# Performance work log

Hardware: AMD Instinct MI355X
Metric: run time of the kernel (lower is better)

## Reference

```python
import jax, jax.numpy as jnp
import numpy as np

N = 100000
C = 128
VEC = 16
GRID = 128
TEMP = 1.0
REP = C // VEC


def _offsets_cube():
    r = [-1, 0, 1]
    return np.array([[i, j, k] for i in r for j in r for k in r], dtype=np.int64)


def _offsets_cross(d):
    offs = [[0, 0, 0]]
    for ax in range(3):
        for s in (-d, d):
            o = [0, 0, 0]
            o[ax] = s
            offs.append(o)
    return np.array(offs, dtype=np.int64)


def _build_nbr(coords, lut, offs):
    # coords [N,3] int, lut: flat grid -> voxel idx or -1. Returns [K,N] int32, -1 = missing.
    maps = []
    for o in offs:
        nc = coords + o
        valid = np.all((nc >= 0) & (nc < GRID), axis=1)
        flat = nc[:, 0] * GRID * GRID + nc[:, 1] * GRID + nc[:, 2]
        idx = np.where(valid, lut[np.clip(flat, 0, GRID ** 3 - 1)], -1)
        maps.append(idx)
    return jnp.asarray(np.stack(maps).astype(np.int32))


def setup_inputs() -> dict:
    rng = np.random.default_rng(0)
    flat = rng.choice(GRID ** 3, size=N, replace=False)
    coords = np.stack([flat // (GRID * GRID), (flat // GRID) % GRID, flat % GRID], axis=1)
    lut = np.full(GRID ** 3, -1, dtype=np.int64)
    lut[flat] = np.arange(N)
    nbr_cross2 = _build_nbr(coords, lut, _offsets_cross(2))  # expert 0: HYPER_CROSS dil=2, K=7
    nbr_cube = _build_nbr(coords, lut, _offsets_cube())       # expert 1: HYPER_CUBE dil=1, K=27
    nbr_cross3 = _build_nbr(coords, lut, _offsets_cross(3))  # expert 2: HYPER_CROSS dil=3, K=7

    ks = jax.random.split(jax.random.key(0), 10)
    s = lambda k, shape, sc: jax.random.normal(k, shape, jnp.float32) * sc
    return dict(
        x=s(ks[0], (N, C), 1.0),
        v1_w=s(ks[1], (27, C, C), 0.05),
        v1_g=jnp.ones((C,), jnp.float32), v1_b=jnp.zeros((C,), jnp.float32),
        v2_w=s(ks[2], (C, C), 0.05),
        v2_g=jnp.ones((C,), jnp.float32), v2_b=jnp.zeros((C,), jnp.float32),
        q_w=s(ks[3], (C, VEC), 0.05),
        q_g=jnp.ones((VEC,), jnp.float32), q_b=jnp.zeros((VEC,), jnp.float32),
        cb0=s(ks[4], (7, C), 0.1),
        cb1=s(ks[5], (27, C), 0.1),
        cb2=s(ks[6], (7, C), 0.1),
        out_w=s(ks[7], (C, C), 0.05),
        out_g=jnp.ones((C,), jnp.float32), out_b=jnp.zeros((C,), jnp.float32),
        nbr_cross2=nbr_cross2, nbr_cube=nbr_cube, nbr_cross3=nbr_cross3,
    )


def _bn(x, g, b, eps=1e-5):
    m = x.mean(0)
    v = x.var(0)
    return (x - m) * jax.lax.rsqrt(v + eps) * g + b


def _sparse_conv(x, nbr, W):
    # full sparse conv: out[i] = sum_k W[k] @ x[nbr[k,i]] over valid neighbors
    out = jnp.zeros((x.shape[0], W.shape[2]), x.dtype)
    for k in range(W.shape[0]):  # fixed small K, structural loop
        idx = nbr[k]
        g = jnp.where((idx >= 0)[:, None], x[jnp.clip(idx, 0)], 0.0)
        out = out + g @ W[k]
    return out


def _chanwise_conv(x, nbr, kern):
    # MinkowskiChannelwiseConvolution: out[i,c] = sum_k kern[k,c] * x[nbr[k,i],c]
    out = jnp.zeros_like(x)
    for k in range(kern.shape[0]):
        idx = nbr[k]
        out = out + jnp.where((idx >= 0)[:, None], x[jnp.clip(idx, 0)], 0.0) * kern[k]
    return out


def _pairwise_score(q, nbr):
    # pairwise qk: mean over valid neighbors j of q_i * q_j (per channel) -> [N, VEC]
    acc = jnp.zeros_like(q)
    cnt = jnp.zeros((q.shape[0], 1), q.dtype)
    for k in range(nbr.shape[0]):
        idx = nbr[k]
        valid = (idx >= 0)[:, None]
        acc = acc + jnp.where(valid, q[jnp.clip(idx, 0)], 0.0)
        cnt = cnt + valid.astype(q.dtype)
    return q * acc / jnp.maximum(cnt, 1.0)


def reference(x, v1_w, v1_g, v1_b, v2_w, v2_g, v2_b, q_w, q_g, q_b,
              cb0, cb1, cb2, out_w, out_g, out_b,
              nbr_cross2, nbr_cube, nbr_cross3):
    # value branch: 3x3 ConvBNReLU -> 1x1 ConvBNReLU
    v = jax.nn.relu(_bn(_sparse_conv(x, nbr_cube, v1_w), v1_g, v1_b))
    v = jax.nn.relu(_bn(v @ v2_w, v2_g, v2_b))
    # query: 1x1 ConvBNReLU -> [N, VEC]
    q = jax.nn.relu(_bn(x @ q_w, q_g, q_b))
    # M=3 channelwise codebook expert convs on the value features
    cb_outs = [
        _chanwise_conv(v, nbr_cross2, cb0),
        _chanwise_conv(v, nbr_cube, cb1),
        _chanwise_conv(v, nbr_cross3, cb2),
    ]
    # pairwise attention scores per expert neighborhood -> [N, VEC, M]
    scores = jnp.stack([
        _pairwise_score(q, nbr_cross2),
        _pairwise_score(q, nbr_cube),
        _pairwise_score(q, nbr_cross3),
    ], axis=-1)
    attn = jax.nn.softmax(scores / TEMP, axis=-1)
    attn = jnp.repeat(attn, REP, axis=1)  # expand_vec_dim: [N, C, M]
    out = sum(attn[:, :, m] * cb_outs[m] for m in range(3))
    out = jax.nn.relu(_bn(out @ out_w, out_g, out_b))
    return out + x  # residual (inplanes == planes, downsample is identity)
```

## Files before the change

kernel.cpp:

```cpp
#include <hip/hip_runtime.h>

#define NN 100000
#define C 128
#define VEC 16
#define AROW 136
#define GCAP 240000

typedef __bf16 bfx8 __attribute__((ext_vector_type(8)));
typedef float f32x4 __attribute__((ext_vector_type(4)));

__device__ inline unsigned pack_bf2(float a, float b) {
    unsigned ua = __float_as_uint(a);
    unsigned ub = __float_as_uint(b);
    ua = (ua + 0x7fffu + ((ua >> 16) & 1u)) >> 16;
    ub = (ub + 0x7fffu + ((ub >> 16) & 1u)) >> 16;
    return ua | (ub << 16);
}
__device__ inline unsigned short bf1(float a) {
    unsigned u = __float_as_uint(a);
    return (unsigned short)((u + 0x7fffu + ((u >> 16) & 1u)) >> 16);
}

__device__ inline void wconv_body(const float* __restrict__ W, unsigned short* __restrict__ Wf, int F) {
    int e = F & 7, l = (F >> 3) & 63, nt = (F >> 9) & 7, ks = (F >> 12) & 3, kt = F >> 14;
    int cin = ks * 32 + (l >> 4) * 8 + e;
    int cout = nt * 16 + (l & 15);
    Wf[F] = bf1(W[((size_t)kt * C + cin) * C + cout]);
}

__global__ __launch_bounds__(256) void prep(const float* __restrict__ v1w, const float* __restrict__ v2w,
                                            const float* __restrict__ outw, const float* __restrict__ x,
                                            unsigned short* __restrict__ v1f, unsigned short* __restrict__ v2f,
                                            unsigned short* __restrict__ outf, unsigned short* __restrict__ xh) {
    int b = blockIdx.x, tid = threadIdx.x;
    if (b < 1728)       wconv_body(v1w, v1f, b * 256 + tid);
    else if (b < 1792)  wconv_body(v2w, v2f, (b - 1728) * 256 + tid);
    else if (b < 1856)  wconv_body(outw, outf, (b - 1792) * 256 + tid);
    else {
        const int total8 = NN * C / 8;
        for (int t = (b - 1856) * 256 + tid; t < total8; t += 1024 * 256) {
            float4 xa = *reinterpret_cast<const float4*>(x + (size_t)t * 8);
            float4 xb = *reinterpret_cast<const float4*>(x + (size_t)t * 8 + 4);
            uint4 pk;
            pk.x = pack_bf2(xa.x, xa.y); pk.y = pack_bf2(xa.z, xa.w);
            pk.z = pack_bf2(xb.x, xb.y); pk.w = pack_bf2(xb.z, xb.w);
            *reinterpret_cast<uint4*>(&xh[(size_t)t * 8]) = pk;
        }
    }
}

__global__ __launch_bounds__(256) void compactA(const int* __restrict__ nbr, int* __restrict__ cnt,
                                                int* __restrict__ slotmap, int* __restrict__ pairs,
                                                unsigned* __restrict__ maskbuf) {
    const int k = blockIdx.x / 49, cb = blockIdx.x % 49, tid = threadIdx.x;
    const int i0 = cb * 2048 + tid * 8;
    int j[8]; int lc = 0;
#pragma unroll
    for (int t = 0; t < 8; ++t) {
        int i = i0 + t;
        j[t] = (i < NN) ? nbr[(size_t)k * NN + i] : -1;
        lc += (j[t] >= 0);
    }
    __shared__ int ls[256]; __shared__ int sbase;
    ls[tid] = lc; __syncthreads();
    for (int off = 1; off < 256; off <<= 1) {
        int v = (tid >= off) ? ls[tid - off] : 0;
        __syncthreads();
        ls[tid] += v;
        __syncthreads();
    }
    if (tid == 255) sbase = atomicAdd(&cnt[k], ls[255]);
    __syncthreads();
    int slot = sbase + ls[tid] - lc;
    for (int t = 0; t < 8; ++t) {
        int i = i0 + t; if (i >= NN) break;
        int s = -1;
        if (j[t] >= 0) {
            s = slot++;
            pairs[(size_t)k * NN + s] = j[t];
            atomicOr(&maskbuf[i], 1u << k);
        }
        slotmap[(size_t)k * NN + i] = s;
    }
}

__global__ void prefixA2(int* __restrict__ hdr) {
    if (threadIdx.x == 0) {
        int co = 0, go = 0;
        for (int k = 0; k < 27; ++k) {
            hdr[32 + k] = co; hdr[64 + k] = go;
            int nch = (hdr[k] + 31) / 32;
            co += nch; go += nch * 32;
        }
        hdr[32 + 27] = co;
    }
}

__global__ __launch_bounds__(256) void convB(const unsigned short* __restrict__ xh, const int* __restrict__ pairs,
                                             const int* __restrict__ hdr, const bfx8* __restrict__ Wf,
                                             unsigned short* __restrict__ g) {
    const int tid = threadIdx.x, l = tid & 63, w = tid >> 6, rr = tid >> 4, gg = tid & 15;
    __shared__ int sco[28], scnt[27], sgo[27];
    __shared__ unsigned short Ash[32 * AROW];
    __shared__ unsigned short Osh[32 * AROW];
    if (tid < 28) sco[tid] = hdr[32 + tid];
    if (tid < 27) { scnt[tid] = hdr[tid]; sgo[tid] = hdr[64 + tid]; }
    __syncthreads();
    const int tot = sco[27];
    for (int t = blockIdx.x; t < tot; t += gridDim.x) {
        int lo = 0, hi = 26;
        while (lo < hi) { int mid = (lo + hi + 1) >> 1; if (sco[mid] <= t) lo = mid; else hi = mid - 1; }
        const int k = lo, c = t - sco[k], cntk = scnt[k];
        const int srow = c * 32;
        const size_t gbase = (size_t)(sgo[k] + srow) * C;
#pragma unroll
        for (int h = 0; h < 2; ++h) {
            int row = srow + h * 16 + rr;
            uint4 pk = {0u, 0u, 0u, 0u};
            if (row < cntk) {
                int j = pairs[(size_t)k * NN + row];
                pk = *reinterpret_cast<const uint4*>(xh + (size_t)j * C + gg * 8);
            }
            *reinterpret_cast<uint4*>(&Ash[(h * 16 + rr) * AROW + gg * 8]) = pk;
        }
        __syncthreads();
        f32x4 a00 = {0.f,0.f,0.f,0.f}, a01 = {0.f,0.f,0.f,0.f};
        f32x4 a10 = {0.f,0.f,0.f,0.f}, a11 = {0.f,0.f,0.f,0.f};
        const unsigned short* ar0 = &Ash[(l & 15) * AROW + (l >> 4) * 8];
        const unsigned short* ar1 = &Ash[(16 + (l & 15)) * AROW + (l >> 4) * 8];
#pragma unroll
        for (int ks = 0; ks < 4; ++ks) {
            bfx8 b0 = Wf[((k * 4 + ks) * 8 + 2 * w) * 64 + l];
            bfx8 b1 = Wf[((k * 4 + ks) * 8 + 2 * w + 1) * 64 + l];
            bfx8 f0 = *reinterpret_cast<const bfx8*>(ar0 + ks * 32);
            bfx8 f1 = *reinterpret_cast<const bfx8*>(ar1 + ks * 32);
            a00 = __builtin_amdgcn_mfma_f32_16x16x32_bf16(f0, b0, a00, 0, 0, 0);
            a01 = __builtin_amdgcn_mfma_f32_16x16x32_bf16(f0, b1, a01, 0, 0, 0);
            a10 = __builtin_amdgcn_mfma_f32_16x16x32_bf16(f1, b0, a10, 0, 0, 0);
            a11 = __builtin_amdgcn_mfma_f32_16x16x32_bf16(f1, b1, a11, 0, 0, 0);
        }
#pragma unroll
        for (int r = 0; r < 4; ++r) {
            int row = (l >> 4) * 4 + r;
            Osh[row * AROW + w * 32 + (l & 15)]        = bf1(a00[r]);
            Osh[row * AROW + w * 32 + 16 + (l & 15)]   = bf1(a01[r]);
            Osh[(16 + row) * AROW + w * 32 + (l & 15)] = bf1(a10[r]);
            Osh[(16 + row) * AROW + w * 32 + 16 + (l & 15)] = bf1(a11[r]);
        }
        __syncthreads();
#pragma unroll
        for (int h = 0; h < 2; ++h) {
            int row = h * 16 + rr;
            uint4 v = *reinterpret_cast<uint4*>(&Osh[row * AROW + gg * 8]);
            *reinterpret_cast<uint4*>(&g[gbase + (size_t)row * C + gg * 8]) = v;
        }
        __syncthreads();
    }
}

__global__ __launch_bounds__(256) void convC(const unsigned short* __restrict__ g, const int* __restrict__ slotmap,
                                             const int* __restrict__ hdr, const unsigned* __restrict__ maskbuf,
                                             unsigned short* __restrict__ outh, float* __restrict__ psb,
                                             float* __restrict__ pqb) {
    const int tid = threadIdx.x, p = tid >> 4, gg = tid & 15, c0 = gg * 8;
    const int i = blockIdx.x * 16 + p;
    __shared__ int sgo[27];
    __shared__ float outt[16 * 132];
    if (tid < 27) sgo[tid] = hdr[64 + tid];
    __syncthreads();
    unsigned m = maskbuf[i];
    float acc[8] = {0.f,0.f,0.f,0.f,0.f,0.f,0.f,0.f};
    while (m) {
        int k = (int)__builtin_ctz(m); m &= m - 1;
        int slot = slotmap[(size_t)k * NN + i];
        const unsigned short* gr = &g[(size_t)(sgo[k] + slot) * C + c0];
        uint4 u = *reinterpret_cast<const uint4*>(gr);
        acc[0] += __uint_as_float(u.x << 16); acc[1] += __uint_as_float(u.x & 0xffff0000u);
        acc[2] += __uint_as_float(u.y << 16); acc[3] += __uint_as_float(u.y & 0xffff0000u);
        acc[4] += __uint_as_float(u.z << 16); acc[5] += __uint_as_float(u.z & 0xffff0000u);
        acc[6] += __uint_as_float(u.w << 16); acc[7] += __uint_as_float(u.w & 0xffff0000u);
    }
#pragma unroll
    for (int c2 = 0; c2 < 8; ++c2) outt[p * 132 + c0 + c2] = acc[c2];
    uint4 pk;
    pk.x = pack_bf2(acc[0], acc[1]); pk.y = pack_bf2(acc[2], acc[3]);
    pk.z = pack_bf2(acc[4], acc[5]); pk.w = pack_bf2(acc[6], acc[7]);
    *reinterpret_cast<uint4*>(&outh[(size_t)i * C + c0]) = pk;
    __syncthreads();
    if (tid < 128) {
        float s = 0.f, q = 0.f;
#pragma unroll
        for (int r = 0; r < 16; ++r) { float v = outt[r * 132 + tid]; s += v; q += v * v; }
        psb[(size_t)blockIdx.x * C + tid] = s;
        pqb[(size_t)blockIdx.x * C + tid] = q;
    }
}

__global__ __launch_bounds__(256) void statsF128(const float* __restrict__ psb, const float* __restrict__ pqb,
                                                 int rows,
                                                 float* __restrict__ ps2, float* __restrict__ pq2,
                                                 const float* __restrict__ g, const float* __restrict__ b,
                                                 float* __restrict__ a, float* __restrict__ cc,
                                                 int* __restrict__ ticket) {
    const int tid = threadIdx.x, ch = tid & 127, half = tid >> 7;
    float s = 0.f, q = 0.f;
    for (int i = blockIdx.x * 2 + half; i < rows; i += 128) {
        s += psb[(size_t)i * C + ch];
        q += pqb[(size_t)i * C + ch];
    }
    __shared__ float ls[256], lq[256];
    __shared__ int amlast;
    ls[tid] = s; lq[tid] = q;
    __syncthreads();
    if (tid < 128) {
        ps2[blockIdx.x * C + ch] = ls[tid] + ls[tid + 128];
        pq2[blockIdx.x * C + ch] = lq[tid] + lq[tid + 128];
    }
    __threadfence();
    __syncthreads();
    if (tid == 0) amlast = (atomicAdd(ticket, 1) == 63) ? 1 : 0;
    __syncthreads();
    if (!amlast) return;
    __threadfence();
    if (tid < 128) {
        float ss = 0.f, qq = 0.f;
        for (int i = 0; i < 64; ++i) { ss += ps2[i * C + ch]; qq += pq2[i * C + ch]; }
        float m = ss / (float)NN;
        float var = fmaxf(qq / (float)NN - m * m, 0.f);
        float rs = rsqrtf(var + 1e-5f);
        float av = g[ch] * rs;
        a[ch] = av;
        cc[ch] = b[ch] - m * av;
    }
}

__global__ __launch_bounds__(256) void statsF16(const float* __restrict__ buf,
                                                float* __restrict__ ps2, float* __restrict__ pq2,
                                                const float* __restrict__ g, const float* __restrict__ b,
                                                float* __restrict__ a, float* __restrict__ cc,
                                                int* __restrict__ ticket) {
    const int tid = threadIdx.x, ch = tid & 15, grp = tid >> 4;
    float s = 0.f, q = 0.f;
    for (int i = blockIdx.x * 16 + grp; i < NN; i += 64 * 16) {
        float val = buf[(size_t)i * VEC + ch];
        s += val; q += val * val;
    }
    __shared__ float ls[256], lq[256];
    __shared__ int amlast;
    ls[tid] = s; lq[tid] = q;
    __syncthreads();
    if (tid < 16) {
        float ss = 0.f, qq = 0.f;
        for (int g2 = 0; g2 < 16; ++g2) { ss += ls[g2 * 16 + ch]; qq += lq[g2 * 16 + ch]; }
        ps2[blockIdx.x * VEC + ch] = ss; pq2[blockIdx.x * VEC + ch] = qq;
    }
    __threadfence();
    __syncthreads();
    if (tid == 0) amlast = (atomicAdd(ticket, 1) == 63) ? 1 : 0;
    __syncthreads();
    if (!amlast) return;
    __threadfence();
    if (tid < 16) {
        float ss = 0.f, qq = 0.f;
        for (int i = 0; i < 64; ++i) { ss += ps2[i * VEC + ch]; qq += pq2[i * VEC + ch]; }
        float m = ss / (float)NN;
        float var = fmaxf(qq / (float)NN - m * m, 0.f);
        float rs = rsqrtf(var + 1e-5f);
        float av = g[ch] * rs;
        a[ch] = av;
        cc[ch] = b[ch] - m * av;
    }
}

__global__ __launch_bounds__(256) void mm_bn_h32(const unsigned short* __restrict__ in,
                                                 const float* __restrict__ a,
                                                 const float* __restrict__ cc,
                                                 int dorelu,
                                                 const bfx8* __restrict__ Wf,
                                                 unsigned short* __restrict__ out,
                                                 float* __restrict__ psb,
                                                 float* __restrict__ pqb) {
    const int tid = threadIdx.x, l = tid & 63, w = tid >> 6;
    const int rr = tid >> 4, gg = tid & 15;
    const size_t base = (size_t)blockIdx.x * 32;
    __shared__ unsigned short Ash[32 * AROW];
    __shared__ float outt[32 * 132];
#pragma unroll
    for (int h = 0; h < 2; ++h) {
        int row = h * 16 + rr;
        uint4 u = *reinterpret_cast<const uint4*>(in + (base + row) * C + gg * 8);
        if (dorelu) {
            float4 a4 = *reinterpret_cast<const float4*>(&a[gg * 8]);
            float4 a4b = *reinterpret_cast<const float4*>(&a[gg * 8 + 4]);
            float4 c4 = *reinterpret_cast<const float4*>(&cc[gg * 8]);
            float4 c4b = *reinterpret_cast<const float4*>(&cc[gg * 8 + 4]);
            float e0 = fmaxf(fmaf(__uint_as_float(u.x << 16),        a4.x,  c4.x), 0.f);
            float e1 = fmaxf(fmaf(__uint_as_float(u.x & 0xffff0000u), a4.y,  c4.y), 0.f);
            float e2 = fmaxf(fmaf(__uint_as_float(u.y << 16),        a4.z,  c4.z), 0.f);
            float e3 = fmaxf(fmaf(__uint_as_float(u.y & 0xffff0000u), a4.w,  c4.w), 0.f);
            float e4 = fmaxf(fmaf(__uint_as_float(u.z << 16),        a4b.x, c4b.x), 0.f);
            float e5 = fmaxf(fmaf(__uint_as_float(u.z & 0xffff0000u), a4b.y, c4b.y), 0.f);
            float e6 = fmaxf(fmaf(__uint_as_float(u.w << 16),        a4b.z, c4b.z), 0.f);
            float e7 = fmaxf(fmaf(__uint_as_float(u.w & 0xffff0000u), a4b.w, c4b.w), 0.f);
            u.x = pack_bf2(e0, e1); u.y = pack_bf2(e2, e3);
            u.z = pack_bf2(e4, e5); u.w = pack_bf2(e6, e7);
        }
        *reinterpret_cast<uint4*>(&Ash[row * AROW + gg * 8]) = u;
    }
    __syncthreads();
    f32x4 a00 = {0.f,0.f,0.f,0.f}, a01 = {0.f,0.f,0.f,0.f};
    f32x4 a10 = {0.f,0.f,0.f,0.f}, a11 = {0.f,0.f,0.f,0.f};
    const unsigned short* ar0 = &Ash[(l & 15) * AROW + (l >> 4) * 8];
    const unsigned short* ar1 = &Ash[(16 + (l & 15)) * AROW + (l >> 4) * 8];
#pragma unroll
    for (int ks = 0; ks < 4; ++ks) {
        bfx8 b0 = Wf[(ks * 8 + 2 * w) * 64 + l];
        bfx8 b1 = Wf[(ks * 8 + 2 * w + 1) * 64 + l];
        bfx8 f0 = *reinterpret_cast<const bfx8*>(ar0 + ks * 32);
        bfx8 f1 = *reinterpret_cast<const bfx8*>(ar1 + ks * 32);
        a00 = __builtin_amdgcn_mfma_f32_16x16x32_bf16(f0, b0, a00, 0, 0, 0);
        a01 = __builtin_amdgcn_mfma_f32_16x16x32_bf16(f0, b1, a01, 0, 0, 0);
        a10 = __builtin_amdgcn_mfma_f32_16x16x32_bf16(f1, b0, a10, 0, 0, 0);
        a11 = __builtin_amdgcn_mfma_f32_16x16x32_bf16(f1, b1, a11, 0, 0, 0);
    }
#pragma unroll
    for (int r = 0; r < 4; ++r) {
        int row = (l >> 4) * 4 + r;
        outt[row * 132 + w * 32 + (l & 15)]        = a00[r];
        outt[row * 132 + w * 32 + 16 + (l & 15)]   = a01[r];
        outt[(16 + row) * 132 + w * 32 + (l & 15)] = a10[r];
        outt[(16 + row) * 132 + w * 32 + 16 + (l & 15)] = a11[r];
    }
    __syncthreads();
#pragma unroll
    for (int h = 0; h < 2; ++h) {
        int row = h * 16 + rr;
        float4 v0 = *reinterpret_cast<float4*>(&outt[row * 132 + gg * 8]);
        float4 v1 = *reinterpret_cast<float4*>(&outt[row * 132 + gg * 8 + 4]);
        uint4 pk;
        pk.x = pack_bf2(v0.x, v0.y); pk.y = pack_bf2(v0.z, v0.w);
        pk.z = pack_bf2(v1.x, v1.y); pk.w = pack_bf2(v1.z, v1.w);
        *reinterpret_cast<uint4*>(&out[(base + row) * C + gg * 8]) = pk;
    }
    if (tid < 128) {
        float s = 0.f, q = 0.f;
#pragma unroll
        for (int r = 0; r < 32; ++r) { float v = outt[r * 132 + tid]; s += v; q += v * v; }
        psb[(size_t)blockIdx.x * C + tid] = s;
        pqb[(size_t)blockIdx.x * C + tid] = q;
    }
}

__global__ __launch_bounds__(256) void qmm(const float* __restrict__ x,
                                           const float* __restrict__ qw,
                                           float* __restrict__ outq) {
    const int v = threadIdx.x & 15, p = threadIdx.x >> 4;
    const size_t i = (size_t)blockIdx.x * 16 + p;
    float acc = 0.f;
    for (int cin0 = 0; cin0 < C; cin0 += 4) {
        float4 xv = *reinterpret_cast<const float4*>(x + i * C + cin0);
        acc += xv.x * qw[(cin0 + 0) * VEC + v] + xv.y * qw[(cin0 + 1) * VEC + v]
             + xv.z * qw[(cin0 + 2) * VEC + v] + xv.w * qw[(cin0 + 3) * VEC + v];
    }
    outq[i * VEC + v] = acc;
}

__global__ __launch_bounds__(256) void attn_fused16e(const unsigned short* __restrict__ vraw,
                                                     const float* __restrict__ a2,
                                                     const float* __restrict__ c2,
                                                     const float* __restrict__ qraw,
                                                     const float* __restrict__ aq,
                                                     const float* __restrict__ cq,
                                                     const int* __restrict__ nA,
                                                     const int* __restrict__ nB,
                                                     const int* __restrict__ nC,
                                                     const float* __restrict__ cb0,
                                                     const float* __restrict__ cb1,
                                                     const float* __restrict__ cb2,
                                                     unsigned short* __restrict__ outm) {
    const int tid = threadIdx.x;
    const int base = blockIdx.x * 16;
    __shared__ int raw[16][41];
    __shared__ int sj[16][44];
    __shared__ short sk[16][44];
    __shared__ short sb[16][4];
    __shared__ float sattn[16][16][3];

    for (int t = tid; t < 656; t += 256) {
        int k = t >> 4, p = t & 15;
        int i = base + p;
        int j;
        if (k < 7)       j = nA[(size_t)k * NN + i];
        else if (k < 34) j = nB[(size_t)(k - 7) * NN + i];
        else             j = nC[(size_t)(k - 34) * NN + i];
        raw[p][k] = j;
    }
    __syncthreads();
    if (tid < 16) {
        int p = tid, n = 0;
#pragma unroll
        for (int k = 0; k < 7; ++k) { int j = raw[p][k]; if (j >= 0) { sj[p][n] = j; sk[p][n] = (short)k; ++n; } }
        int b0 = n;
#pragma unroll
        for (int k = 7; k < 34; ++k) { int j = raw[p][k]; if (j >= 0) { sj[p][n] = j; sk[p][n] = (short)(k - 7); ++n; } }
        int b1 = n;
#pragma unroll
        for (int k = 34; k < 41; ++k) { int j = raw[p][k]; if (j >= 0) { sj[p][n] = j; sk[p][n] = (short)(k - 34); ++n; } }
        sb[p][0] = (short)b0; sb[p][1] = (short)b1; sb[p][2] = (short)n;
    }
    __syncthreads();
    {
        int p = tid >> 4, v = tid & 15;
        int b0 = sb[p][0], b1 = sb[p][1], b2 = sb[p][2];
        float av = aq[v], cv = cq[v];
        float qi = fmaxf(fmaf(qraw[(size_t)(base + p) * VEC + v], av, cv), 0.f);
        float a0 = 0.f, a1 = 0.f, a2s = 0.f;
        for (int s = 0; s < b0; ++s) a0 += fmaxf(fmaf(qraw[(size_t)sj[p][s] * VEC + v], av, cv), 0.f);
        for (int s = b0; s < b1; ++s) a1 += fmaxf(fmaf(qraw[(size_t)sj[p][s] * VEC + v], av, cv), 0.f);
        for (int s = b1; s < b2; ++s) a2s += fmaxf(fmaf(qraw[(size_t)sj[p][s] * VEC + v], av, cv), 0.f);
        float s0 = qi * a0 / (float)(b0 > 0 ? b0 : 1);
        float s1 = qi * a1 / (float)(b1 - b0 > 0 ? b1 - b0 : 1);
        float s2 = qi * a2s / (float)(b2 - b1 > 0 ? b2 - b1 : 1);
        float mx = fmaxf(s0, fmaxf(s1, s2));
        float e0 = __expf(s0 - mx), e1 = __expf(s1 - mx), e2 = __expf(s2 - mx);
        float inv = 1.f / (e0 + e1 + e2);
        sattn[p][v][0] = e0 * inv; sattn[p][v][1] = e1 * inv; sattn[p][v][2] = e2 * inv;
    }
    __syncthreads();
    {
        int p = tid >> 4, g = tid & 15, c0 = g * 8;
        int b0 = sb[p][0], b1 = sb[p][1], b2 = sb[p][2];
        float4 va = *reinterpret_cast<const float4*>(&a2[c0]);
        float4 vab = *reinterpret_cast<const float4*>(&a2[c0 + 4]);
        float4 vc = *reinterpret_cast<const float4*>(&c2[c0]);
        float4 vcb = *reinterpret_cast<const float4*>(&c2[c0 + 4]);
        float A0[8], A1[8], A2[8];
#pragma unroll
        for (int c = 0; c < 8; ++c) { A0[c] = 0.f; A1[c] = 0.f; A2[c] = 0.f; }
        for (int s = 0; s < b0; ++s) {
            int j = sj[p][s], k = sk[p][s];
            uint4 u = *reinterpret_cast<const uint4*>(vraw + (size_t)j * C + c0);
            float4 ca = *reinterpret_cast<const float4*>(&cb0[k * C + c0]);
            float4 cb = *reinterpret_cast<const float4*>(&cb0[k * C + c0 + 4]);
            A0[0] = fmaf(ca.x, fmaxf(fmaf(__uint_as_float(u.x << 16),        va.x,  vc.x), 0.f), A0[0]);
            A0[1] = fmaf(ca.y, fmaxf(fmaf(__uint_as_float(u.x & 0xffff0000u), va.y,  vc.y), 0.f), A0[1]);
            A0[2] = fmaf(ca.z, fmaxf(fmaf(__uint_as_float(u.y << 16),        va.z,  vc.z), 0.f), A0[2]);
            A0[3] = fmaf(ca.w, fmaxf(fmaf(__uint_as_float(u.y & 0xffff0000u), va.w,  vc.w), 0.f), A0[3]);
            A0[4] = fmaf(cb.x, fmaxf(fmaf(__uint_as_float(u.z << 16),        vab.x, vcb.x), 0.f), A0[4]);
            A0[5] = fmaf(cb.y, fmaxf(fmaf(__uint_as_float(u.z & 0xffff0000u), vab.y, vcb.y), 0.f), A0[5]);
            A0[6] = fmaf(cb.z, fmaxf(fmaf(__uint_as_float(u.w << 16),        vab.z, vcb.z), 0.f), A0[6]);
            A0[7] = fmaf(cb.w, fmaxf(fmaf(__uint_as_float(u.w & 0xffff0000u), vab.w, vcb.w), 0.f), A0[7]);
        }
        for (int s = b0; s < b1; ++s) {
            int j = sj[p][s], k = sk[p][s];
            uint4 u = *reinterpret_cast<const uint4*>(vraw + (size_t)j * C + c0);
            float4 ca = *reinterpret_cast<const float4*>(&cb1[k * C + c0]);
            float4 cb = *reinterpret_cast<const float4*>(&cb1[k * C + c0 + 4]);
            A1[0] = fmaf(ca.x, fmaxf(fmaf(__uint_as_float(u.x << 16),        va.x,  vc.x), 0.f), A1[0]);
            A1[1] = fmaf(ca.y, fmaxf(fmaf(__uint_as_float(u.x & 0xffff0000u), va.y,  vc.y), 0.f), A1[1]);
            A1[2] = fmaf(ca.z, fmaxf(fmaf(__uint_as_float(u.y << 16),        va.z,  vc.z), 0.f), A1[2]);
            A1[3] = fmaf(ca.w, fmaxf(fmaf(__uint_as_float(u.y & 0xffff0000u), va.w,  vc.w), 0.f), A1[3]);
            A1[4] = fmaf(cb.x, fmaxf(fmaf(__uint_as_float(u.z << 16),        vab.x, vcb.x), 0.f), A1[4]);
            A1[5] = fmaf(cb.y, fmaxf(fmaf(__uint_as_float(u.z & 0xffff0000u), vab.y, vcb.y), 0.f), A1[5]);
            A1[6] = fmaf(cb.z, fmaxf(fmaf(__uint_as_float(u.w << 16),        vab.z, vcb.z), 0.f), A1[6]);
            A1[7] = fmaf(cb.w, fmaxf(fmaf(__uint_as_float(u.w & 0xffff0000u), vab.w, vcb.w), 0.f), A1[7]);
        }
        for (int s = b1; s < b2; ++s) {
            int j = sj[p][s], k = sk[p][s];
            uint4 u = *reinterpret_cast<const uint4*>(vraw + (size_t)j * C + c0);
            float4 ca = *reinterpret_cast<const float4*>(&cb2[k * C + c0]);
            float4 cb = *reinterpret_cast<const float4*>(&cb2[k * C + c0 + 4]);
            A2[0] = fmaf(ca.x, fmaxf(fmaf(__uint_as_float(u.x << 16),        va.x,  vc.x), 0.f), A2[0]);
            A2[1] = fmaf(ca.y, fmaxf(fmaf(__uint_as_float(u.x & 0xffff0000u), va.y,  vc.y), 0.f), A2[1]);
            A2[2] = fmaf(ca.z, fmaxf(fmaf(__uint_as_float(u.y << 16),        va.z,  vc.z), 0.f), A2[2]);
            A2[3] = fmaf(ca.w, fmaxf(fmaf(__uint_as_float(u.y & 0xffff0000u), va.w,  vc.w), 0.f), A2[3]);
            A2[4] = fmaf(cb.x, fmaxf(fmaf(__uint_as_float(u.z << 16),        vab.x, vcb.x), 0.f), A2[4]);
            A2[5] = fmaf(cb.y, fmaxf(fmaf(__uint_as_float(u.z & 0xffff0000u), vab.y, vcb.y), 0.f), A2[5]);
            A2[6] = fmaf(cb.z, fmaxf(fmaf(__uint_as_float(u.w << 16),        vab.z, vcb.z), 0.f), A2[6]);
            A2[7] = fmaf(cb.w, fmaxf(fmaf(__uint_as_float(u.w & 0xffff0000u), vab.w, vcb.w), 0.f), A2[7]);
        }
        float w0 = sattn[p][g][0], w1 = sattn[p][g][1], w2 = sattn[p][g][2];
        float o[8];
#pragma unroll
        for (int c = 0; c < 8; ++c) o[c] = w0 * A0[c] + w1 * A1[c] + w2 * A2[c];
        uint4 pk;
        pk.x = pack_bf2(o[0], o[1]); pk.y = pack_bf2(o[2], o[3]);
        pk.z = pack_bf2(o[4], o[5]); pk.w = pack_bf2(o[6], o[7]);
        *reinterpret_cast<uint4*>(&outm[(size_t)(base + p) * C + c0]) = pk;
    }
}

__global__ __launch_bounds__(256) void final_bn_res_h(const unsigned short* __restrict__ buf,
                                                      const float* __restrict__ a,
                                                      const float* __restrict__ cc,
                                                      const float* __restrict__ x,
                                                      float* __restrict__ out) {
    const int total8 = NN * C / 8;
    for (int t = blockIdx.x * 256 + threadIdx.x; t < total8; t += gridDim.x * 256) {
        int ch = (t * 8) & 127;
        uint4 u = *reinterpret_cast<const uint4*>(buf + (size_t)t * 8);
        float4 xa = *reinterpret_cast<const float4*>(x + (size_t)t * 8);
        float4 xb = *reinterpret_cast<const float4*>(x + (size_t)t * 8 + 4);
        float4 a4 = *reinterpret_cast<const float4*>(&a[ch]);
        float4 a4b = *reinterpret_cast<const float4*>(&a[ch + 4]);
        float4 c4 = *reinterpret_cast<const float4*>(&cc[ch]);
        float4 c4b = *reinterpret_cast<const float4*>(&cc[ch + 4]);
        float4 o0, o1;
        o0.x = fmaxf(fmaf(__uint_as_float(u.x << 16),        a4.x,  c4.x), 0.f) + xa.x;
        o0.y = fmaxf(fmaf(__uint_as_float(u.x & 0xffff0000u), a4.y,  c4.y), 0.f) + xa.y;
        o0.z = fmaxf(fmaf(__uint_as_float(u.y << 16),        a4.z,  c4.z), 0.f) + xa.z;
        o0.w = fmaxf(fmaf(__uint_as_float(u.y & 0xffff0000u), a4.w,  c4.w), 0.f) + xa.w;
        o1.x = fmaxf(fmaf(__uint_as_float(u.z << 16),        a4b.x, c4b.x), 0.f) + xb.x;
        o1.y = fmaxf(fmaf(__uint_as_float(u.z & 0xffff0000u), a4b.y, c4b.y), 0.f) + xb.y;
        o1.z = fmaxf(fmaf(__uint_as_float(u.w << 16),        a4b.z, c4b.z), 0.f) + xb.z;
        o1.w = fmaxf(fmaf(__uint_as_float(u.w & 0xffff0000u), a4b.w, c4b.w), 0.f) + xb.w;
        *reinterpret_cast<float4*>(out + (size_t)t * 8) = o0;
        *reinterpret_cast<float4*>(out + (size_t)t * 8 + 4) = o1;
    }
}

extern "C" void kernel_launch(void* const* d_in, const int* in_sizes, int n_in,
                              void* d_out, int out_size, void* d_ws, size_t ws_size,
                              hipStream_t stream) {
    (void)in_sizes; (void)n_in; (void)out_size; (void)ws_size;
    const float* x    = (const float*)d_in[0];
    const float* v1_w = (const float*)d_in[1];
    const float* v1_g = (const float*)d_in[2];
    const float* v1_b = (const float*)d_in[3];
    const float* v2_w = (const float*)d_in[4];
    const float* v2_g = (const float*)d_in[5];
    const float* v2_b = (const float*)d_in[6];
    const float* q_w  = (const float*)d_in[7];
    const float* q_g  = (const float*)d_in[8];
    const float* q_b  = (const float*)d_in[9];
    const float* cb0  = (const float*)d_in[10];
    const float* cb1  = (const float*)d_in[11];
    const float* cb2  = (const float*)d_in[12];
    const float* out_w = (const float*)d_in[13];
    const float* out_g = (const float*)d_in[14];
    const float* out_b = (const float*)d_in[15];
    const int* nbrA = (const int*)d_in[16];
    const int* nbrB = (const int*)d_in[17];
    const int* nbrC = (const int*)d_in[18];
    float* out = (float*)d_out;

    float* w = (float*)d_ws;
    unsigned short* bufAh = (unsigned short*)w;
    float* r1 = w + (size_t)NN * C / 2;
    unsigned short* g = (unsigned short*)r1;
    int* slotmap = (int*)(r1 + 15360000);
    int* pairs   = (int*)(r1 + 15360000 + 2700000);
    unsigned short* bufBh = (unsigned short*)r1;
    float* bufQ = r1 + 6400000;
    size_t o = (size_t)NN * C / 2 + 20760000;
    unsigned short* xh = (unsigned short*)(w + o); o += (size_t)NN * C / 2;
    float* psb  = w + o; o += (size_t)6250 * C;
    float* pqb  = w + o; o += (size_t)6250 * C;
    float* ps2  = w + o; o += 64 * C;
    float* pq2  = w + o; o += 64 * C;
    float* ps16 = w + o; o += 64 * VEC;
    float* pq16 = w + o; o += 64 * VEC;
    float* a1 = w + o; o += C;  float* c1 = w + o; o += C;
    float* a2 = w + o; o += C;  float* c2 = w + o; o += C;
    float* ao = w + o; o += C;  float* co = w + o; o += C;
    float* aq = w + o; o += VEC; float* cq = w + o; o += VEC;
    unsigned short* v1f = (unsigned short*)(w + o); o += (27 * 16384) / 2;
    unsigned short* v2f = (unsigned short*)(w + o); o += 16384 / 2;
    unsigned short* outf = (unsigned short*)(w + o); o += 16384 / 2;
    int* hdr = (int*)(w + o); o += 128;
    unsigned* maskbuf = (unsigned*)(w + o); o += NN;

    hipMemsetAsync(hdr, 0, (size_t)(128 + NN) * sizeof(int), stream);
    prep<<<2880, 256, 0, stream>>>(v1_w, v2_w, out_w, x, v1f, v2f, outf, xh);

    compactA<<<27 * 49, 256, 0, stream>>>(nbrB, hdr, slotmap, pairs, maskbuf);
    prefixA2<<<1, 64, 0, stream>>>(hdr);
    convB<<<2048, 256, 0, stream>>>(xh, pairs, hdr, (const bfx8*)v1f, g);
    convC<<<NN / 16, 256, 0, stream>>>(g, slotmap, hdr, maskbuf, bufAh, psb, pqb);
    statsF128<<<64, 256, 0, stream>>>(psb, pqb, 6250, ps2, pq2, v1_g, v1_b, a1, c1, hdr + 96);

    mm_bn_h32<<<NN / 32, 256, 0, stream>>>(bufAh, a1, c1, 1, (const bfx8*)v2f, bufBh, psb, pqb);
    statsF128<<<64, 256, 0, stream>>>(psb, pqb, 3125, ps2, pq2, v2_g, v2_b, a2, c2, hdr + 97);

    qmm<<<NN / 16, 256, 0, stream>>>(x, q_w, bufQ);
    statsF16<<<64, 256, 0, stream>>>(bufQ, ps16, pq16, q_g, q_b, aq, cq, hdr + 98);

    attn_fused16e<<<NN / 16, 256, 0, stream>>>(bufBh, a2, c2, bufQ, aq, cq,
                                               nbrA, nbrB, nbrC, cb0, cb1, cb2, bufAh);

    mm_bn_h32<<<NN / 32, 256, 0, stream>>>(bufAh, nullptr, nullptr, 0, (const bfx8*)outf, bufBh, psb, pqb);
    statsF128<<<64, 256, 0, stream>>>(psb, pqb, 3125, ps2, pq2, out_g, out_b, ao, co, hdr + 99);
    final_bn_res_h<<<2048, 256, 0, stream>>>(bufBh, ao, co, x, out);
}
```

Measured before the change: 338.0 us.

## Fuse output projection into attention kernel and fold prefix scan into compaction

The attention-mix kernel now multiplies its 16-row output tile by the output projection weights with MFMA and emits per-block BN partial sums directly. This removes the separate output matmul launch and the bf16 round-trip of the mixed features through global memory. The prefix computation over per-offset counts moves into the last-finishing compaction block via an atomic counter, and the query projection reads the bf16 copy of x instead of fp32. The costs are more shared memory per attention block, which may lower occupancy, and extra bf16 rounding of x in the query path.

```diff
diff --git a/kernel.cpp b/kernel.cpp
--- a/kernel.cpp
+++ b/kernel.cpp
@@ -49,7 +49,7 @@
     }
 }
 
-__global__ __launch_bounds__(256) void compactA(const int* __restrict__ nbr, int* __restrict__ cnt,
+__global__ __launch_bounds__(256) void compactA(const int* __restrict__ nbr, int* __restrict__ hdr,
                                                 int* __restrict__ slotmap, int* __restrict__ pairs,
                                                 unsigned* __restrict__ maskbuf) {
     const int k = blockIdx.x / 49, cb = blockIdx.x % 49, tid = threadIdx.x;
@@ -61,7 +61,7 @@
         j[t] = (i < NN) ? nbr[(size_t)k * NN + i] : -1;
         lc += (j[t] >= 0);
     }
-    __shared__ int ls[256]; __shared__ int sbase;
+    __shared__ int ls[256]; __shared__ int sbase; __shared__ int amlast;
     ls[tid] = lc; __syncthreads();
     for (int off = 1; off < 256; off <<= 1) {
         int v = (tid >= off) ? ls[tid - off] : 0;
@@ -69,7 +69,7 @@
         ls[tid] += v;
         __syncthreads();
     }
-    if (tid == 255) sbase = atomicAdd(&cnt[k], ls[255]);
+    if (tid == 255) sbase = atomicAdd(&hdr[k], ls[255]);
     __syncthreads();
     int slot = sbase + ls[tid] - lc;
     for (int t = 0; t < 8; ++t) {
@@ -82,17 +82,20 @@
         }
         slotmap[(size_t)k * NN + i] = s;
     }
-}
-
-__global__ void prefixA2(int* __restrict__ hdr) {
-    if (threadIdx.x == 0) {
+    __threadfence();
+    __syncthreads();
+    if (tid == 0) amlast = (atomicAdd(&hdr[100], 1) == 27 * 49 - 1) ? 1 : 0;
+    __syncthreads();
+    if (amlast && tid == 0) {
         int co = 0, go = 0;
-        for (int k = 0; k < 27; ++k) {
-            hdr[32 + k] = co; hdr[64 + k] = go;
-            int nch = (hdr[k] + 31) / 32;
+        for (int kk = 0; kk < 27; ++kk) {
+            int cnt = atomicAdd(&hdr[kk], 0);
+            hdr[32 + kk] = co; hdr[64 + kk] = go;
+            int nch = (cnt + 31) / 32;
             co += nch; go += nch * 32;
         }
         hdr[32 + 27] = co;
+        __threadfence();
     }
 }
 
@@ -275,7 +278,6 @@
 __global__ __launch_bounds__(256) void mm_bn_h32(const unsigned short* __restrict__ in,
                                                  const float* __restrict__ a,
                                                  const float* __restrict__ cc,
-                                                 int dorelu,
                                                  const bfx8* __restrict__ Wf,
                                                  unsigned short* __restrict__ out,
                                                  float* __restrict__ psb,
@@ -285,26 +287,24 @@
     const size_t base = (size_t)blockIdx.x * 32;
     __shared__ unsigned short Ash[32 * AROW];
     __shared__ float outt[32 * 132];
+    float4 a4 = *reinterpret_cast<const float4*>(&a[gg * 8]);
+    float4 a4b = *reinterpret_cast<const float4*>(&a[gg * 8 + 4]);
+    float4 c4 = *reinterpret_cast<const float4*>(&cc[gg * 8]);
+    float4 c4b = *reinterpret_cast<const float4*>(&cc[gg * 8 + 4]);
 #pragma unroll
     for (int h = 0; h < 2; ++h) {
         int row = h * 16 + rr;
         uint4 u = *reinterpret_cast<const uint4*>(in + (base + row) * C + gg * 8);
-        if (dorelu) {
-            float4 a4 = *reinterpret_cast<const float4*>(&a[gg * 8]);
-            float4 a4b = *reinterpret_cast<const float4*>(&a[gg * 8 + 4]);
-            float4 c4 = *reinterpret_cast<const float4*>(&cc[gg * 8]);
-            float4 c4b = *reinterpret_cast<const float4*>(&cc[gg * 8 + 4]);
-            float e0 = fmaxf(fmaf(__uint_as_float(u.x << 16),        a4.x,  c4.x), 0.f);
-            float e1 = fmaxf(fmaf(__uint_as_float(u.x & 0xffff0000u), a4.y,  c4.y), 0.f);
-            float e2 = fmaxf(fmaf(__uint_as_float(u.y << 16),        a4.z,  c4.z), 0.f);
-            float e3 = fmaxf(fmaf(__uint_as_float(u.y & 0xffff0000u), a4.w,  c4.w), 0.f);
-            float e4 = fmaxf(fmaf(__uint_as_float(u.z << 16),        a4b.x, c4b.x), 0.f);
-            float e5 = fmaxf(fmaf(__uint_as_float(u.z & 0xffff0000u), a4b.y, c4b.y), 0.f);
-            float e6 = fmaxf(fmaf(__uint_as_float(u.w << 16),        a4b.z, c4b.z), 0.f);
-            float e7 = fmaxf(fmaf(__uint_as_float(u.w & 0xffff0000u), a4b.w, c4b.w), 0.f);
-            u.x = pack_bf2(e0, e1); u.y = pack_bf2(e2, e3);
-            u.z = pack_bf2(e4, e5); u.w = pack_bf2(e6, e7);
-        }
+        float e0 = fmaxf(fmaf(__uint_as_float(u.x << 16),        a4.x,  c4.x), 0.f);
+        float e1 = fmaxf(fmaf(__uint_as_float(u.x & 0xffff0000u), a4.y,  c4.y), 0.f);
+        float e2 = fmaxf(fmaf(__uint_as_float(u.y << 16),        a4.z,  c4.z), 0.f);
+        float e3 = fmaxf(fmaf(__uint_as_float(u.y & 0xffff0000u), a4.w,  c4.w), 0.f);
+        float e4 = fmaxf(fmaf(__uint_as_float(u.z << 16),        a4b.x, c4b.x), 0.f);
+        float e5 = fmaxf(fmaf(__uint_as_float(u.z & 0xffff0000u), a4b.y, c4b.y), 0.f);
+        float e6 = fmaxf(fmaf(__uint_as_float(u.w << 16),        a4b.z, c4b.z), 0.f);
+        float e7 = fmaxf(fmaf(__uint_as_float(u.w & 0xffff0000u), a4b.w, c4b.w), 0.f);
+        u.x = pack_bf2(e0, e1); u.y = pack_bf2(e2, e3);
+        u.z = pack_bf2(e4, e5); u.w = pack_bf2(e6, e7);
         *reinterpret_cast<uint4*>(&Ash[row * AROW + gg * 8]) = u;
     }
     __syncthreads();
@@ -351,40 +351,51 @@
     }
 }
 
-__global__ __launch_bounds__(256) void qmm(const float* __restrict__ x,
-                                           const float* __restrict__ qw,
-                                           float* __restrict__ outq) {
+__global__ __launch_bounds__(256) void qmmh(const unsigned short* __restrict__ xh,
+                                            const float* __restrict__ qw,
+                                            float* __restrict__ outq) {
     const int v = threadIdx.x & 15, p = threadIdx.x >> 4;
     const size_t i = (size_t)blockIdx.x * 16 + p;
     float acc = 0.f;
-    for (int cin0 = 0; cin0 < C; cin0 += 4) {
-        float4 xv = *reinterpret_cast<const float4*>(x + i * C + cin0);
-        acc += xv.x * qw[(cin0 + 0) * VEC + v] + xv.y * qw[(cin0 + 1) * VEC + v]
-             + xv.z * qw[(cin0 + 2) * VEC + v] + xv.w * qw[(cin0 + 3) * VEC + v];
+    for (int cin0 = 0; cin0 < C; cin0 += 8) {
+        uint4 u = *reinterpret_cast<const uint4*>(xh + i * C + cin0);
+        acc += __uint_as_float(u.x << 16)         * qw[(cin0 + 0) * VEC + v]
+             + __uint_as_float(u.x & 0xffff0000u) * qw[(cin0 + 1) * VEC + v]
+             + __uint_as_float(u.y << 16)         * qw[(cin0 + 2) * VEC + v]
+             + __uint_as_float(u.y & 0xffff0000u) * qw[(cin0 + 3) * VEC + v]
+             + __uint_as_float(u.z << 16)         * qw[(cin0 + 4) * VEC + v]
+             + __uint_as_float(u.z & 0xffff0000u) * qw[(cin0 + 5) * VEC + v]
+             + __uint_as_float(u.w << 16)         * qw[(cin0 + 6) * VEC + v]
+             + __uint_as_float(u.w & 0xffff0000u) * qw[(cin0 + 7) * VEC + v];
     }
     outq[i * VEC + v] = acc;
 }
 
-__global__ __launch_bounds__(256) void attn_fused16e(const unsigned short* __restrict__ vraw,
-                                                     const float* __restrict__ a2,
-                                                     const float* __restrict__ c2,
-                                                     const float* __restrict__ qraw,
-                                                     const float* __restrict__ aq,
-                                                     const float* __restrict__ cq,
-                                                     const int* __restrict__ nA,
-                                                     const int* __restrict__ nB,
-                                                     const int* __restrict__ nC,
-                                                     const float* __restrict__ cb0,
-                                                     const float* __restrict__ cb1,
-                                                     const float* __restrict__ cb2,
-                                                     unsigned short* __restrict__ outm) {
-    const int tid = threadIdx.x;
+__global__ __launch_bounds__(256) void attn_out(const unsigned short* __restrict__ vraw,
+                                                const float* __restrict__ a2,
+                                                const float* __restrict__ c2,
+                                                const float* __restrict__ qraw,
+                                                const float* __restrict__ aq,
+                                                const float* __restrict__ cq,
+                                                const int* __restrict__ nA,
+                                                const int* __restrict__ nB,
+                                                const int* __restrict__ nC,
+                                                const float* __restrict__ cb0,
+                                                const float* __restrict__ cb1,
+                                                const float* __restrict__ cb2,
+                                                const bfx8* __restrict__ Wf,
+                                                unsigned short* __restrict__ outh,
+                                                float* __restrict__ psb,
+                                                float* __restrict__ pqb) {
+    const int tid = threadIdx.x, l = tid & 63, w = tid >> 6;
     const int base = blockIdx.x * 16;
     __shared__ int raw[16][41];
     __shared__ int sj[16][44];
     __shared__ short sk[16][44];
     __shared__ short sb[16][4];
     __shared__ float sattn[16][16][3];
+    __shared__ unsigned short Ash[16 * AROW];
+    __shared__ float outt[16 * 132];
 
     for (int t = tid; t < 656; t += 256) {
         int k = t >> 4, p = t & 15;
@@ -486,7 +497,44 @@
         uint4 pk;
         pk.x = pack_bf2(o[0], o[1]); pk.y = pack_bf2(o[2], o[3]);
         pk.z = pack_bf2(o[4], o[5]); pk.w = pack_bf2(o[6], o[7]);
-        *reinterpret_cast<uint4*>(&outm[(size_t)(base + p) * C + c0]) = pk;
+        *reinterpret_cast<uint4*>(&Ash[p * AROW + c0]) = pk;
+    }
+    __syncthreads();
+    {
+        f32x4 acc0 = {0.f, 0.f, 0.f, 0.f};
+        f32x4 acc1 = {0.f, 0.f, 0.f, 0.f};
+        const unsigned short* arow = &Ash[(l & 15) * AROW + (l >> 4) * 8];
+#pragma unroll
+        for (int ks = 0; ks < 4; ++ks) {
+            bfx8 af = *reinterpret_cast<const bfx8*>(arow + ks * 32);
+            bfx8 b0 = Wf[(ks * 8 + 2 * w) * 64 + l];
+            bfx8 b1 = Wf[(ks * 8 + 2 * w + 1) * 64 + l];
+            acc0 = __builtin_amdgcn_mfma_f32_16x16x32_bf16(af, b0, acc0, 0, 0, 0);
+            acc1 = __builtin_amdgcn_mfma_f32_16x16x32_bf16(af, b1, acc1, 0, 0, 0);
+        }
+#pragma unroll
+        for (int r = 0; r < 4; ++r) {
+            int row = (l >> 4) * 4 + r;
+            outt[row * 132 + w * 32 + (l & 15)] = acc0[r];
+            outt[row * 132 + w * 32 + 16 + (l & 15)] = acc1[r];
+        }
+    }
+    __syncthreads();
+    {
+        int rr = tid >> 4, gg = tid & 15;
+        float4 v0 = *reinterpret_cast<float4*>(&outt[rr * 132 + gg * 8]);
+        float4 v1 = *reinterpret_cast<float4*>(&outt[rr * 132 + gg * 8 + 4]);
+        uint4 pk;
+        pk.x = pack_bf2(v0.x, v0.y); pk.y = pack_bf2(v0.z, v0.w);
+        pk.z = pack_bf2(v1.x, v1.y); pk.w = pack_bf2(v1.z, v1.w);
+        *reinterpret_cast<uint4*>(&outh[(size_t)(base + rr) * C + gg * 8]) = pk;
+    }
+    if (tid < 128) {
+        float s = 0.f, q = 0.f;
+#pragma unroll
+        for (int r = 0; r < 16; ++r) { float v = outt[r * 132 + tid]; s += v; q += v * v; }
+        psb[(size_t)blockIdx.x * C + tid] = s;
+        pqb[(size_t)blockIdx.x * C + tid] = q;
     }
 }
 
@@ -574,21 +622,20 @@
     prep<<<2880, 256, 0, stream>>>(v1_w, v2_w, out_w, x, v1f, v2f, outf, xh);
 
     compactA<<<27 * 49, 256, 0, stream>>>(nbrB, hdr, slotmap, pairs, maskbuf);
-    prefixA2<<<1, 64, 0, stream>>>(hdr);
     convB<<<2048, 256, 0, stream>>>(xh, pairs, hdr, (const bfx8*)v1f, g);
     convC<<<NN / 16, 256, 0, stream>>>(g, slotmap, hdr, maskbuf, bufAh, psb, pqb);
     statsF128<<<64, 256, 0, stream>>>(psb, pqb, 6250, ps2, pq2, v1_g, v1_b, a1, c1, hdr + 96);
 
-    mm_bn_h32<<<NN / 32, 256, 0, stream>>>(bufAh, a1, c1, 1, (const bfx8*)v2f, bufBh, psb, pqb);
+    mm_bn_h32<<<NN / 32, 256, 0, stream>>>(bufAh, a1, c1, (const bfx8*)v2f, bufBh, psb, pqb);
     statsF128<<<64, 256, 0, stream>>>(psb, pqb, 3125, ps2, pq2, v2_g, v2_b, a2, c2, hdr + 97);
 
-    qmm<<<NN / 16, 256, 0, stream>>>(x, q_w, bufQ);
+    qmmh<<<NN / 16, 256, 0, stream>>>(xh, q_w, bufQ);
     statsF16<<<64, 256, 0, stream>>>(bufQ, ps16, pq16, q_g, q_b, aq, cq, hdr + 98);
 
-    attn_fused16e<<<NN / 16, 256, 0, stream>>>(bufBh, a2, c2, bufQ, aq, cq,
-                                               nbrA, nbrB, nbrC, cb0, cb1, cb2, bufAh);
-
-    mm_bn_h32<<<NN / 32, 256, 0, stream>>>(bufAh, nullptr, nullptr, 0, (const bfx8*)outf, bufBh, psb, pqb);
-    statsF128<<<64, 256, 0, stream>>>(psb, pqb, 3125, ps2, pq2, out_g, out_b, ao, co, hdr + 99);
-    final_bn_res_h<<<2048, 256, 0, stream>>>(bufBh, ao, co, x, out);
-}
+    attn_out<<<NN / 16, 256, 0, stream>>>(bufBh, a2, c2, bufQ, aq, cq,
+                                          nbrA, nbrB, nbrC, cb0, cb1, cb2,
+                                          (const bfx8*)outf, bufAh, psb, pqb);
+    statsF128<<<64, 256, 0, stream>>>(psb, pqb, 6250, ps2, pq2, out_g, out_b, ao, co, hdr + 99);
+
+    final_bn_res_h<<<2048, 256, 0, stream>>>(bufAh, ao, co, x, out);
+}
```

Result: slower. 527.9 us (+56.2%).
